# Performance work log

Hardware: AMD Instinct MI355X
Metric: run time of the kernel (lower is better)

## Reference

```python
import jax, jax.numpy as jnp
import numpy as np

N, E, FN, FE, H, L, S = 50000, 800000, 16, 8, 64, 3, 32

def layernorm(h, g, b, eps=1e-5):
    mu = h.mean(-1, keepdims=True)
    var = ((h - mu) ** 2).mean(-1, keepdims=True)
    return (h - mu) / jnp.sqrt(var + eps) * g + b

def setup_inputs() -> dict:
    key = jax.random.key(0)
    ks = iter(jax.random.split(key, 64))
    nrm = lambda shape: jax.random.normal(next(ks), shape, jnp.float32) * 0.05
    inp = {}
    inp['x'] = jax.random.normal(next(ks), (N, FN), jnp.float32)
    inp['edge_index'] = jax.random.randint(next(ks), (2, E), 0, N)
    inp['edge_attr'] = jax.random.normal(next(ks), (E, FE), jnp.float32)
    # node / edge encoders: Linear -> ReLU -> LayerNorm
    inp['Wn'] = nrm((FN, H)); inp['bn'] = jnp.zeros((H,)); inp['gn'] = jnp.ones((H,)); inp['betan'] = jnp.zeros((H,))
    inp['We'] = nrm((FE, H)); inp['be'] = jnp.zeros((H,)); inp['ge'] = jnp.ones((H,)); inp['betae'] = jnp.zeros((H,))
    # EdgeConv MLPs (stacked over layers): Linear(2H,H) -> ReLU -> Linear(H,H)
    inp['Wc1'] = nrm((L, 2 * H, H)); inp['bc1'] = jnp.zeros((L, H))
    inp['Wc2'] = nrm((L, H, H)); inp['bc2'] = jnp.zeros((L, H))
    # GATConv (heads=1): lin weight, att_src, att_dst, bias
    inp['Wg'] = nrm((L, H, H)); inp['att_src'] = nrm((L, H)); inp['att_dst'] = nrm((L, H)); inp['bg'] = jnp.zeros((L, H))
    # q predictor
    inp['Wq1'] = nrm((H, H)); inp['bq1'] = jnp.zeros((H,)); inp['gq'] = jnp.ones((H,)); inp['betaq'] = jnp.zeros((H,))
    inp['Wq2'] = nrm((H, S)); inp['bq2'] = jnp.zeros((S,))
    # value predictor
    inp['Wv1'] = nrm((H, H)); inp['bv1'] = jnp.zeros((H,)); inp['gv'] = jnp.ones((H,)); inp['betav'] = jnp.zeros((H,))
    inp['Wv2'] = nrm((H, 1)); inp['bv2'] = jnp.zeros((1,))
    return inp

def reference(x, edge_index, edge_attr, Wn, bn, gn, betan, We, be, ge, betae,
              Wc1, bc1, Wc2, bc2, Wg, att_src, att_dst, bg,
              Wq1, bq1, gq, betaq, Wq2, bq2, Wv1, bv1, gv, betav, Wv2, bv2):
    n = x.shape[0]
    src, dst = edge_index[0], edge_index[1]  # PyG: row=source(j), col=target(i)
    h = layernorm(jax.nn.relu(x @ Wn + bn), gn, betan)
    _ea = layernorm(jax.nn.relu(edge_attr @ We + be), ge, betae)  # encoded but unused by EdgeConv message (faithful)
    loop = jnp.arange(n)
    gsrc = jnp.concatenate([src, loop])  # GAT adds self-loops
    gdst = jnp.concatenate([dst, loop])
    for l in range(L):
        # EdgeConv: gather x_i (target), x_j (source), concat, MLP, scatter-max at target
        m = jnp.concatenate([h[dst], h[src]], axis=1)  # [E, 2H]
        m = jax.nn.relu(m @ Wc1[l] + bc1[l]) @ Wc2[l] + bc2[l]
        agg = jax.ops.segment_max(m, dst, num_segments=n)
        agg = jnp.where(jnp.isneginf(agg), 0.0, agg)  # PyG scatter-max leaves empty rows at 0
        # GATConv (1 head): alpha = softmax_i(leaky_relu(a_s.xg_j + a_d.xg_i))
        xg = h @ Wg[l]
        a_s = xg @ att_src[l]
        a_d = xg @ att_dst[l]
        e = jax.nn.leaky_relu(a_s[gsrc] + a_d[gdst], 0.2)
        emax = jax.ops.segment_max(e, gdst, num_segments=n)
        w = jnp.exp(e - emax[gdst])
        alpha = w / jax.ops.segment_sum(w, gdst, num_segments=n)[gdst]
        att = jax.ops.segment_sum(xg[gsrc] * alpha[:, None], gdst, num_segments=n) + bg[l]
        h = jax.nn.relu(h + agg + att)
    t = h[0]
    tq = layernorm(jax.nn.relu(t @ Wq1 + bq1), gq, betaq)
    q_values = tq @ Wq2 + bq2
    tv = layernorm(jax.nn.relu(t @ Wv1 + bv1), gv, betav)
    value = tv @ Wv2 + bv2
    return (q_values, value)
```

## Files before the change

kernel.cpp:

```cpp
#include <hip/hip_runtime.h>
#include <math.h>

#define N_NODES 50000
#define N_EDGES 800000
#define FN_DIM 16
#define HD 64
#define T_CAP 8192
#define T2_CAP 512
#define MAXDEG 128

__device__ __forceinline__ float wsum64(float v) {
    #pragma unroll
    for (int o = 1; o < 64; o <<= 1) v += __shfl_xor(v, o);
    return v;
}
__device__ __forceinline__ float wmax64(float v) {
    #pragma unroll
    for (int o = 1; o < 64; o <<= 1) v = fmaxf(v, __shfl_xor(v, o));
    return v;
}
__device__ __forceinline__ float lrelu02(float v) { return v > 0.f ? v : 0.2f * v; }

__global__ void k_mark2(const int* __restrict__ ei, int* need1, int* need2) {
    int e = blockIdx.x * blockDim.x + threadIdx.x;
    if (e == 0) { need1[0] = 1; need2[0] = 1; }
    if (e >= N_EDGES) return;
    if (ei[N_EDGES + e] == 0) { int s = ei[e]; need2[s] = 1; need1[s] = 1; }
}
__global__ void k_mark1(const int* __restrict__ ei, const int* __restrict__ need2, int* need1) {
    int e = blockIdx.x * blockDim.x + threadIdx.x;
    if (e >= N_EDGES) return;
    if (need2[ei[N_EDGES + e]]) need1[ei[e]] = 1;
}
__global__ void k_compact(const int* __restrict__ need1, const int* __restrict__ need2,
                          int* list1, int* list2, int* idx1, int* idx2, int* cnt) {
    int i = blockIdx.x * blockDim.x + threadIdx.x;
    if (i >= N_NODES) return;
    if (need1[i]) { int p = atomicAdd(&cnt[0], 1); if (p < T_CAP)  { list1[p] = i; idx1[i] = p; } }
    if (need2[i]) { int p = atomicAdd(&cnt[1], 1); if (p < T2_CAP) { list2[p] = i; idx2[i] = p; } }
}
__global__ void k_bucket(const int* __restrict__ ei, const int* __restrict__ need1,
                         const int* __restrict__ need2,
                         const int* __restrict__ idx1, const int* __restrict__ idx2,
                         int* eb1, int* deg1, int* eb2, int* deg2, int* eb3, int* deg3) {
    int e = blockIdx.x * blockDim.x + threadIdx.x;
    if (e >= N_EDGES) return;
    int d = ei[N_EDGES + e];
    int s = ei[e];
    if (need1[d]) {
        int t = idx1[d];
        if ((unsigned)t < T_CAP) { int p = atomicAdd(&deg1[t], 1); if (p < MAXDEG) eb1[t * MAXDEG + p] = s; }
    }
    if (need2[d]) {
        int t = idx2[d];
        if ((unsigned)t < T2_CAP) { int p = atomicAdd(&deg2[t], 1); if (p < MAXDEG) eb2[t * MAXDEG + p] = s; }
    }
    if (d == 0) { int p = atomicAdd(deg3, 1); if (p < MAXDEG) eb3[p] = s; }
}

template<int LM>
__device__ __forceinline__ float node_h(int i, int lane,
    const float* __restrict__ x, const float* __restrict__ Wn, const float* __restrict__ bn,
    const float* __restrict__ gn, const float* __restrict__ betan,
    const float* __restrict__ hin) {
    if (LM == 0) {
        float acc = bn[lane];
        #pragma unroll
        for (int k = 0; k < FN_DIM; k++) acc += x[i * FN_DIM + k] * Wn[k * HD + lane];
        float v = fmaxf(acc, 0.f);
        float mu = wsum64(v) * (1.f / 64.f);
        float d = v - mu;
        float var = wsum64(d * d) * (1.f / 64.f);
        return d * rsqrtf(var + 1e-5f) * gn[lane] + betan[lane];
    } else {
        return hin[i * HD + lane];
    }
}

__device__ __forceinline__ void heads_eval(float hv, int lane,
    const float* __restrict__ Wq1, const float* __restrict__ bq1,
    const float* __restrict__ gq, const float* __restrict__ betaq,
    const float* __restrict__ Wq2, const float* __restrict__ bq2,
    const float* __restrict__ Wv1, const float* __restrict__ bv1,
    const float* __restrict__ gv, const float* __restrict__ betav,
    const float* __restrict__ Wv2, const float* __restrict__ bv2,
    float* __restrict__ out) {
    float acc = bq1[lane];
    #pragma unroll 8
    for (int k = 0; k < 64; k++) acc += __shfl(hv, k) * Wq1[k * 64 + lane];
    float r = fmaxf(acc, 0.f);
    float mu = wsum64(r) * (1.f / 64.f);
    float d = r - mu;
    float var = wsum64(d * d) * (1.f / 64.f);
    float tq = d * rsqrtf(var + 1e-5f) * gq[lane] + betaq[lane];
    float accv = bv1[lane];
    #pragma unroll 8
    for (int k = 0; k < 64; k++) accv += __shfl(hv, k) * Wv1[k * 64 + lane];
    float rv = fmaxf(accv, 0.f);
    float muv = wsum64(rv) * (1.f / 64.f);
    float dv = rv - muv;
    float varv = wsum64(dv * dv) * (1.f / 64.f);
    float tv = dv * rsqrtf(varv + 1e-5f) * gv[lane] + betav[lane];
    int s = lane & 31;
    float q = bq2[s];
    #pragma unroll 8
    for (int k = 0; k < 64; k++) q += __shfl(tq, k) * Wq2[k * 32 + s];
    if (lane < 32) out[lane] = q;
    float vsum = wsum64(tv * Wv2[lane]);
    if (lane == 0) out[32] = vsum + bv2[0];
}

template<int LM>
__global__ __launch_bounds__(256) void k_layer(
    const float* __restrict__ x, const float* __restrict__ Wn, const float* __restrict__ bn,
    const float* __restrict__ gn, const float* __restrict__ betan,
    const float* __restrict__ hin,
    const float* __restrict__ Wc1, const float* __restrict__ bc1,
    const float* __restrict__ Wc2, const float* __restrict__ bc2,
    const float* __restrict__ Wg, const float* __restrict__ atts, const float* __restrict__ attd,
    const float* __restrict__ bgv,
    const int* __restrict__ tlist, const int* __restrict__ cntp, int tcap,
    const int* __restrict__ eb, const int* __restrict__ deg,
    float* __restrict__ hout,
    const float* __restrict__ Wq1, const float* __restrict__ bq1,
    const float* __restrict__ gq, const float* __restrict__ betaq,
    const float* __restrict__ Wq2, const float* __restrict__ bq2,
    const float* __restrict__ Wv1, const float* __restrict__ bv1,
    const float* __restrict__ gv, const float* __restrict__ betav,
    const float* __restrict__ Wv2, const float* __restrict__ bv2)
{
    __shared__ float ht[64], ut[64], xgt[64];
    __shared__ float scr[4][4][64];
    __shared__ float xgc[MAXDEG][64];
    __shared__ float ec[MAXDEG];
    __shared__ float redA[4][64], redB[4][64];
    __shared__ float sws[4];
    __shared__ float sA[2];
    __shared__ float sEm;

    int lane = threadIdx.x & 63;
    int wv = threadIdx.x >> 6;
    int ntgt = (LM == 2) ? 1 : min(cntp[0], tcap);

    for (int w = blockIdx.x; w < ntgt; w += gridDim.x) {
        int t = (LM == 2) ? 0 : tlist[w];
        if (wv == 0) {
            float h = node_h<LM>(t, lane, x, Wn, bn, gn, betan, hin);
            ht[lane] = h;
            float u = bc1[lane], xg = 0.f;
            #pragma unroll 4
            for (int k = 0; k < 64; k++) {
                float b = ht[k];
                u  += b * Wc1[k * 64 + lane];
                xg += b * Wg[k * 64 + lane];
            }
            ut[lane] = u; xgt[lane] = xg;
            float a_st = wsum64(xg * atts[lane]);
            float a_dt = wsum64(xg * attd[lane]);
            if (lane == 0) { sA[0] = a_st; sA[1] = a_dt; }
        }
        __syncthreads();
        int dg = deg[(LM == 2) ? 0 : w]; if (dg > MAXDEG) dg = MAXDEG;
        float a_dt = sA[1];
        float aggw = -INFINITY;

        for (int base = wv * 4; base < dg; base += 16) {
            int ne = dg - base; if (ne > 4) ne = 4;
            #pragma unroll
            for (int e = 0; e < 4; e++) {
                if (e < ne) {
                    int s = eb[w * MAXDEG + base + e];
                    scr[wv][e][lane] = node_h<LM>(s, lane, x, Wn, bn, gn, betan, hin);
                }
            }
            float v[4] = {0.f, 0.f, 0.f, 0.f};
            float g[4] = {0.f, 0.f, 0.f, 0.f};
            #pragma unroll 4
            for (int k = 0; k < 64; k++) {
                float wc = Wc1[(64 + k) * 64 + lane];
                float wg = Wg[k * 64 + lane];
                #pragma unroll
                for (int e = 0; e < 4; e++) {
                    float b = scr[wv][e][k];
                    v[e] += b * wc;
                    g[e] += b * wg;
                }
            }
            float ut_l = ut[lane];
            #pragma unroll
            for (int e = 0; e < 4; e++) scr[wv][e][lane] = fmaxf(ut_l + v[e], 0.f);
            float m[4];
            #pragma unroll
            for (int e = 0; e < 4; e++) m[e] = bc2[lane];
            #pragma unroll 4
            for (int k = 0; k < 64; k++) {
                float wc2v = Wc2[k * 64 + lane];
                #pragma unroll
                for (int e = 0; e < 4; e++) m[e] += scr[wv][e][k] * wc2v;
            }
            #pragma unroll
            for (int e = 0; e < 4; e++) {
                if (e < ne) {
                    aggw = fmaxf(aggw, m[e]);
                    int j = base + e;
                    xgc[j][lane] = g[e];
                    float a_ss = wsum64(g[e] * atts[lane]);
                    if (lane == 0) ec[j] = lrelu02(a_ss + a_dt);
                }
            }
        }
        redA[wv][lane] = aggw;
        __syncthreads();

        if (wv == 0) {
            float es = lrelu02(sA[0] + sA[1]);
            float mm = es;
            for (int j = lane; j < dg; j += 64) mm = fmaxf(mm, ec[j]);
            mm = wmax64(mm);
            if (lane == 0) sEm = mm;
        }
        __syncthreads();
        float em = sEm;
        float attv = 0.f, wsv = 0.f;
        for (int j = wv; j < dg; j += 4) {
            float wj = expf(ec[j] - em);
            attv += wj * xgc[j][lane];
            wsv += wj;
        }
        redB[wv][lane] = attv;
        if (lane == 0) sws[wv] = wsv;
        __syncthreads();

        if (wv == 0) {
            float agg = fmaxf(fmaxf(redA[0][lane], redA[1][lane]),
                              fmaxf(redA[2][lane], redA[3][lane]));
            if (dg == 0) agg = 0.f;
            float es = lrelu02(sA[0] + sA[1]);
            float wself = expf(es - em);
            float att = redB[0][lane] + redB[1][lane] + redB[2][lane] + redB[3][lane]
                      + wself * xgt[lane];
            float wsum = sws[0] + sws[1] + sws[2] + sws[3] + wself;
            float hv = fmaxf(ht[lane] + agg + att / wsum + bgv[lane], 0.f);
            if (LM == 2) {
                heads_eval(hv, lane, Wq1, bq1, gq, betaq, Wq2, bq2,
                           Wv1, bv1, gv, betav, Wv2, bv2, hout);
            } else {
                hout[t * HD + lane] = hv;
            }
        }
        __syncthreads();
    }
}

extern "C" void kernel_launch(void* const* d_in, const int* in_sizes, int n_in,
                              void* d_out, int out_size, void* d_ws, size_t ws_size,
                              hipStream_t stream) {
    const float* x        = (const float*)d_in[0];
    const int*   ei       = (const int*)d_in[1];
    const float* Wn       = (const float*)d_in[3];
    const float* bn       = (const float*)d_in[4];
    const float* gn       = (const float*)d_in[5];
    const float* betan    = (const float*)d_in[6];
    const float* Wc1      = (const float*)d_in[11];
    const float* bc1      = (const float*)d_in[12];
    const float* Wc2      = (const float*)d_in[13];
    const float* bc2      = (const float*)d_in[14];
    const float* Wg       = (const float*)d_in[15];
    const float* att_src  = (const float*)d_in[16];
    const float* att_dst  = (const float*)d_in[17];
    const float* bg       = (const float*)d_in[18];
    const float* Wq1      = (const float*)d_in[19];
    const float* bq1      = (const float*)d_in[20];
    const float* gq       = (const float*)d_in[21];
    const float* betaq    = (const float*)d_in[22];
    const float* Wq2      = (const float*)d_in[23];
    const float* bq2      = (const float*)d_in[24];
    const float* Wv1      = (const float*)d_in[25];
    const float* bv1      = (const float*)d_in[26];
    const float* gv       = (const float*)d_in[27];
    const float* betav    = (const float*)d_in[28];
    const float* Wv2      = (const float*)d_in[29];
    const float* bv2      = (const float*)d_in[30];

    float* hB   = (float*)d_ws;
    float* hA   = hB + (size_t)N_NODES * HD;
    int* need1  = (int*)(hA + (size_t)N_NODES * HD);
    int* need2  = need1 + N_NODES;
    int* deg1   = need2 + N_NODES;
    int* deg2   = deg1 + T_CAP;
    int* deg3   = deg2 + T2_CAP;
    int* cnt    = deg3 + 4;
    int* idx1   = cnt + 8;
    int* idx2   = idx1 + N_NODES;
    int* list1  = idx2 + N_NODES;
    int* list2  = list1 + T_CAP;
    int* eb1    = list2 + T2_CAP;
    int* eb2    = eb1 + (size_t)T_CAP * MAXDEG;
    int* eb3    = eb2 + (size_t)T2_CAP * MAXDEG;

    size_t zero_ints = (size_t)2 * N_NODES + T_CAP + T2_CAP + 12;
    hipMemsetAsync(need1, 0, zero_ints * sizeof(int), stream);

    const int EB = (N_EDGES + 255) / 256;
    const int NB = (N_NODES + 255) / 256;

    k_mark2<<<EB, 256, 0, stream>>>(ei, need1, need2);
    k_mark1<<<EB, 256, 0, stream>>>(ei, need2, need1);
    k_compact<<<NB, 256, 0, stream>>>(need1, need2, list1, list2, idx1, idx2, cnt);
    k_bucket<<<EB, 256, 0, stream>>>(ei, need1, need2, idx1, idx2,
                                     eb1, deg1, eb2, deg2, eb3, deg3);

    k_layer<0><<<512, 256, 0, stream>>>(
        x, Wn, bn, gn, betan, (const float*)nullptr,
        Wc1 + 0 * 2 * HD * HD, bc1 + 0 * HD, Wc2 + 0 * HD * HD, bc2 + 0 * HD,
        Wg + 0 * HD * HD, att_src + 0 * HD, att_dst + 0 * HD, bg + 0 * HD,
        list1, cnt + 0, T_CAP, eb1, deg1, hB,
        Wq1, bq1, gq, betaq, Wq2, bq2, Wv1, bv1, gv, betav, Wv2, bv2);

    k_layer<1><<<64, 256, 0, stream>>>(
        x, Wn, bn, gn, betan, hB,
        Wc1 + 1 * 2 * HD * HD, bc1 + 1 * HD, Wc2 + 1 * HD * HD, bc2 + 1 * HD,
        Wg + 1 * HD * HD, att_src + 1 * HD, att_dst + 1 * HD, bg + 1 * HD,
        list2, cnt + 1, T2_CAP, eb2, deg2, hA,
        Wq1, bq1, gq, betaq, Wq2, bq2, Wv1, bv1, gv, betav, Wv2, bv2);

    k_layer<2><<<1, 256, 0, stream>>>(
        x, Wn, bn, gn, betan, hA,
        Wc1 + 2 * 2 * HD * HD, bc1 + 2 * HD, Wc2 + 2 * HD * HD, bc2 + 2 * HD,
        Wg + 2 * HD * HD, att_src + 2 * HD, att_dst + 2 * HD, bg + 2 * HD,
        (const int*)nullptr, cnt + 1, 1, eb3, deg3, (float*)d_out,
        Wq1, bq1, gq, betaq, Wq2, bq2, Wv1, bv1, gv, betav, Wv2, bv2);
}
```

Baseline: 98.36 us.

## Fold GAT projection after attention aggregation and vectorize graph preprocessing

```diff
diff --git a/kernel.cpp b/kernel.cpp
--- a/kernel.cpp
+++ b/kernel.cpp
@@ -21,52 +21,89 @@
 }
 __device__ __forceinline__ float lrelu02(float v) { return v > 0.f ? v : 0.2f * v; }
 
+__global__ void k_zero(int4* __restrict__ p, int n4) {
+    int i = blockIdx.x * blockDim.x + threadIdx.x;
+    if (i < n4) p[i] = make_int4(0, 0, 0, 0);
+}
+
 __global__ void k_mark2(const int* __restrict__ ei, int* need1, int* need2) {
-    int e = blockIdx.x * blockDim.x + threadIdx.x;
-    if (e == 0) { need1[0] = 1; need2[0] = 1; }
-    if (e >= N_EDGES) return;
-    if (ei[N_EDGES + e] == 0) { int s = ei[e]; need2[s] = 1; need1[s] = 1; }
+    int i = blockIdx.x * blockDim.x + threadIdx.x;
+    if (i == 0) { need1[0] = 1; need2[0] = 1; }
+    if (i >= N_EDGES / 4) return;
+    int4 d4 = ((const int4*)(ei + N_EDGES))[i];
+    int4 s4 = ((const int4*)ei)[i];
+    if (d4.x == 0) { need2[s4.x] = 1; need1[s4.x] = 1; }
+    if (d4.y == 0) { need2[s4.y] = 1; need1[s4.y] = 1; }
+    if (d4.z == 0) { need2[s4.z] = 1; need1[s4.z] = 1; }
+    if (d4.w == 0) { need2[s4.w] = 1; need1[s4.w] = 1; }
 }
 __global__ void k_mark1(const int* __restrict__ ei, const int* __restrict__ need2, int* need1) {
-    int e = blockIdx.x * blockDim.x + threadIdx.x;
-    if (e >= N_EDGES) return;
-    if (need2[ei[N_EDGES + e]]) need1[ei[e]] = 1;
-}
+    int i = blockIdx.x * blockDim.x + threadIdx.x;
+    if (i >= N_EDGES / 4) return;
+    int4 d4 = ((const int4*)(ei + N_EDGES))[i];
+    int4 s4 = ((const int4*)ei)[i];
+    if (need2[d4.x]) need1[s4.x] = 1;
+    if (need2[d4.y]) need1[s4.y] = 1;
+    if (need2[d4.z]) need1[s4.z] = 1;
+    if (need2[d4.w]) need1[s4.w] = 1;
+}
+
 __global__ void k_compact(const int* __restrict__ need1, const int* __restrict__ need2,
-                          int* list1, int* list2, int* idx1, int* idx2, int* cnt) {
-    int i = blockIdx.x * blockDim.x + threadIdx.x;
-    if (i >= N_NODES) return;
-    if (need1[i]) { int p = atomicAdd(&cnt[0], 1); if (p < T_CAP)  { list1[p] = i; idx1[i] = p; } }
-    if (need2[i]) { int p = atomicAdd(&cnt[1], 1); if (p < T2_CAP) { list2[p] = i; idx2[i] = p; } }
-}
+                          int* list1, int* list2, int* idx1, int* idx2, int* cnt,
+                          const float* __restrict__ Wg, const float* __restrict__ atts,
+                          const float* __restrict__ attd, float* __restrict__ pvec) {
+    int i = blockIdx.x * blockDim.x + threadIdx.x;
+    if (i < N_NODES) {
+        if (need1[i]) { int p = atomicAdd(&cnt[0], 1); if (p < T_CAP)  { list1[p] = i; idx1[i] = p; } }
+        if (need2[i]) { int p = atomicAdd(&cnt[1], 1); if (p < T2_CAP) { list2[p] = i; idx2[i] = p; } }
+    }
+    if (blockIdx.x < 6 && threadIdx.x < 64) {
+        int task = blockIdx.x; int l = task >> 1; int which = task & 1;
+        const float* att = which ? attd : atts;
+        float av = att[l * 64 + threadIdx.x];
+        const float* wg = Wg + l * 4096 + threadIdx.x * 64;
+        float acc = 0.f;
+        #pragma unroll 8
+        for (int c = 0; c < 64; c++) acc += wg[c] * __shfl(av, c);
+        pvec[l * 128 + which * 64 + threadIdx.x] = acc;
+    }
+}
+
 __global__ void k_bucket(const int* __restrict__ ei, const int* __restrict__ need1,
                          const int* __restrict__ need2,
                          const int* __restrict__ idx1, const int* __restrict__ idx2,
                          int* eb1, int* deg1, int* eb2, int* deg2, int* eb3, int* deg3) {
-    int e = blockIdx.x * blockDim.x + threadIdx.x;
-    if (e >= N_EDGES) return;
-    int d = ei[N_EDGES + e];
-    int s = ei[e];
-    if (need1[d]) {
-        int t = idx1[d];
-        if ((unsigned)t < T_CAP) { int p = atomicAdd(&deg1[t], 1); if (p < MAXDEG) eb1[t * MAXDEG + p] = s; }
-    }
-    if (need2[d]) {
-        int t = idx2[d];
-        if ((unsigned)t < T2_CAP) { int p = atomicAdd(&deg2[t], 1); if (p < MAXDEG) eb2[t * MAXDEG + p] = s; }
-    }
-    if (d == 0) { int p = atomicAdd(deg3, 1); if (p < MAXDEG) eb3[p] = s; }
+    int i = blockIdx.x * blockDim.x + threadIdx.x;
+    if (i >= N_EDGES / 4) return;
+    int4 d4 = ((const int4*)(ei + N_EDGES))[i];
+    int4 s4 = ((const int4*)ei)[i];
+    int ds[4] = {d4.x, d4.y, d4.z, d4.w};
+    int ss[4] = {s4.x, s4.y, s4.z, s4.w};
+    #pragma unroll
+    for (int c = 0; c < 4; c++) {
+        int d = ds[c], s = ss[c];
+        if (need1[d]) {
+            int t = idx1[d];
+            if ((unsigned)t < T_CAP) { int p = atomicAdd(&deg1[t], 1); if (p < MAXDEG) eb1[t * MAXDEG + p] = s; }
+        }
+        if (need2[d]) {
+            int t = idx2[d];
+            if ((unsigned)t < T2_CAP) { int p = atomicAdd(&deg2[t], 1); if (p < MAXDEG) eb2[t * MAXDEG + p] = s; }
+        }
+        if (d == 0) { int p = atomicAdd(deg3, 1); if (p < MAXDEG) eb3[p] = s; }
+    }
 }
 
 template<int LM>
-__device__ __forceinline__ float node_h(int i, int lane,
+__device__ __forceinline__ float node_h1(int i, int lane,
     const float* __restrict__ x, const float* __restrict__ Wn, const float* __restrict__ bn,
     const float* __restrict__ gn, const float* __restrict__ betan,
     const float* __restrict__ hin) {
     if (LM == 0) {
+        float xv = x[i * FN_DIM + (lane & 15)];
         float acc = bn[lane];
         #pragma unroll
-        for (int k = 0; k < FN_DIM; k++) acc += x[i * FN_DIM + k] * Wn[k * HD + lane];
+        for (int k = 0; k < FN_DIM; k++) acc += __shfl(xv, k) * Wn[k * HD + lane];
         float v = fmaxf(acc, 0.f);
         float mu = wsum64(v) * (1.f / 64.f);
         float d = v - mu;
@@ -77,47 +114,14 @@
     }
 }
 
-__device__ __forceinline__ void heads_eval(float hv, int lane,
-    const float* __restrict__ Wq1, const float* __restrict__ bq1,
-    const float* __restrict__ gq, const float* __restrict__ betaq,
-    const float* __restrict__ Wq2, const float* __restrict__ bq2,
-    const float* __restrict__ Wv1, const float* __restrict__ bv1,
-    const float* __restrict__ gv, const float* __restrict__ betav,
-    const float* __restrict__ Wv2, const float* __restrict__ bv2,
-    float* __restrict__ out) {
-    float acc = bq1[lane];
-    #pragma unroll 8
-    for (int k = 0; k < 64; k++) acc += __shfl(hv, k) * Wq1[k * 64 + lane];
-    float r = fmaxf(acc, 0.f);
-    float mu = wsum64(r) * (1.f / 64.f);
-    float d = r - mu;
-    float var = wsum64(d * d) * (1.f / 64.f);
-    float tq = d * rsqrtf(var + 1e-5f) * gq[lane] + betaq[lane];
-    float accv = bv1[lane];
-    #pragma unroll 8
-    for (int k = 0; k < 64; k++) accv += __shfl(hv, k) * Wv1[k * 64 + lane];
-    float rv = fmaxf(accv, 0.f);
-    float muv = wsum64(rv) * (1.f / 64.f);
-    float dv = rv - muv;
-    float varv = wsum64(dv * dv) * (1.f / 64.f);
-    float tv = dv * rsqrtf(varv + 1e-5f) * gv[lane] + betav[lane];
-    int s = lane & 31;
-    float q = bq2[s];
-    #pragma unroll 8
-    for (int k = 0; k < 64; k++) q += __shfl(tq, k) * Wq2[k * 32 + s];
-    if (lane < 32) out[lane] = q;
-    float vsum = wsum64(tv * Wv2[lane]);
-    if (lane == 0) out[32] = vsum + bv2[0];
-}
-
 template<int LM>
-__global__ __launch_bounds__(256) void k_layer(
+__global__ __launch_bounds__(256, 1) void k_layer(
     const float* __restrict__ x, const float* __restrict__ Wn, const float* __restrict__ bn,
     const float* __restrict__ gn, const float* __restrict__ betan,
     const float* __restrict__ hin,
     const float* __restrict__ Wc1, const float* __restrict__ bc1,
     const float* __restrict__ Wc2, const float* __restrict__ bc2,
-    const float* __restrict__ Wg, const float* __restrict__ atts, const float* __restrict__ attd,
+    const float* __restrict__ Wg, const float* __restrict__ pvec,
     const float* __restrict__ bgv,
     const int* __restrict__ tlist, const int* __restrict__ cntp, int tcap,
     const int* __restrict__ eb, const int* __restrict__ deg,
@@ -129,91 +133,95 @@
     const float* __restrict__ gv, const float* __restrict__ betav,
     const float* __restrict__ Wv2, const float* __restrict__ bv2)
 {
-    __shared__ float ht[64], ut[64], xgt[64];
-    __shared__ float scr[4][4][64];
-    __shared__ float xgc[MAXDEG][64];
+    __shared__ float hsc[MAXDEG][HD];
     __shared__ float ec[MAXDEG];
-    __shared__ float redA[4][64], redB[4][64];
+    __shared__ float redA[4][HD];
+    __shared__ float redH[4][HD];
     __shared__ float sws[4];
-    __shared__ float sA[2];
+    __shared__ float sOut[HD];
     __shared__ float sEm;
 
     int lane = threadIdx.x & 63;
     int wv = threadIdx.x >> 6;
     int ntgt = (LM == 2) ? 1 : min(cntp[0], tcap);
+    float ps = pvec[lane], pd = pvec[64 + lane];
 
     for (int w = blockIdx.x; w < ntgt; w += gridDim.x) {
         int t = (LM == 2) ? 0 : tlist[w];
-        if (wv == 0) {
-            float h = node_h<LM>(t, lane, x, Wn, bn, gn, betan, hin);
-            ht[lane] = h;
-            float u = bc1[lane], xg = 0.f;
-            #pragma unroll 4
-            for (int k = 0; k < 64; k++) {
-                float b = ht[k];
-                u  += b * Wc1[k * 64 + lane];
-                xg += b * Wg[k * 64 + lane];
-            }
-            ut[lane] = u; xgt[lane] = xg;
-            float a_st = wsum64(xg * atts[lane]);
-            float a_dt = wsum64(xg * attd[lane]);
-            if (lane == 0) { sA[0] = a_st; sA[1] = a_dt; }
-        }
-        __syncthreads();
+        float hval = node_h1<LM>(t, lane, x, Wn, bn, gn, betan, hin);
+        float uval = bc1[lane];
+        #pragma unroll 8
+        for (int k = 0; k < HD; k++) uval += __shfl(hval, k) * Wc1[k * HD + lane];
+        float a_st = wsum64(hval * ps);
+        float a_dt = wsum64(hval * pd);
+        float es = lrelu02(a_st + a_dt);
+
         int dg = deg[(LM == 2) ? 0 : w]; if (dg > MAXDEG) dg = MAXDEG;
-        float a_dt = sA[1];
         float aggw = -INFINITY;
 
         for (int base = wv * 4; base < dg; base += 16) {
             int ne = dg - base; if (ne > 4) ne = 4;
+            float hs[4] = {0.f, 0.f, 0.f, 0.f};
+            if (LM == 0) {
+                float xv[4] = {0.f, 0.f, 0.f, 0.f};
+                #pragma unroll
+                for (int e = 0; e < 4; e++)
+                    if (e < ne) xv[e] = x[eb[w * MAXDEG + base + e] * FN_DIM + (lane & 15)];
+                #pragma unroll
+                for (int e = 0; e < 4; e++) hs[e] = bn[lane];
+                #pragma unroll
+                for (int k = 0; k < FN_DIM; k++) {
+                    float wn = Wn[k * HD + lane];
+                    #pragma unroll
+                    for (int e = 0; e < 4; e++) hs[e] += __shfl(xv[e], k) * wn;
+                }
+                #pragma unroll
+                for (int e = 0; e < 4; e++) {
+                    float v = fmaxf(hs[e], 0.f);
+                    float mu = wsum64(v) * (1.f / 64.f);
+                    float d = v - mu;
+                    float var = wsum64(d * d) * (1.f / 64.f);
+                    hs[e] = d * rsqrtf(var + 1e-5f) * gn[lane] + betan[lane];
+                }
+            } else {
+                #pragma unroll
+                for (int e = 0; e < 4; e++)
+                    if (e < ne) hs[e] = hin[eb[w * MAXDEG + base + e] * HD + lane];
+            }
             #pragma unroll
             for (int e = 0; e < 4; e++) {
                 if (e < ne) {
-                    int s = eb[w * MAXDEG + base + e];
-                    scr[wv][e][lane] = node_h<LM>(s, lane, x, Wn, bn, gn, betan, hin);
+                    hsc[base + e][lane] = hs[e];
+                    float as = wsum64(hs[e] * ps);
+                    if (lane == 0) ec[base + e] = lrelu02(as + a_dt);
                 }
             }
             float v[4] = {0.f, 0.f, 0.f, 0.f};
-            float g[4] = {0.f, 0.f, 0.f, 0.f};
-            #pragma unroll 4
-            for (int k = 0; k < 64; k++) {
-                float wc = Wc1[(64 + k) * 64 + lane];
-                float wg = Wg[k * 64 + lane];
-                #pragma unroll
-                for (int e = 0; e < 4; e++) {
-                    float b = scr[wv][e][k];
-                    v[e] += b * wc;
-                    g[e] += b * wg;
-                }
-            }
-            float ut_l = ut[lane];
+            #pragma unroll 8
+            for (int k = 0; k < HD; k++) {
+                float wc = Wc1[(HD + k) * HD + lane];
+                #pragma unroll
+                for (int e = 0; e < 4; e++) v[e] += __shfl(hs[e], k) * wc;
+            }
+            float hid[4];
             #pragma unroll
-            for (int e = 0; e < 4; e++) scr[wv][e][lane] = fmaxf(ut_l + v[e], 0.f);
+            for (int e = 0; e < 4; e++) hid[e] = fmaxf(uval + v[e], 0.f);
             float m[4];
             #pragma unroll
             for (int e = 0; e < 4; e++) m[e] = bc2[lane];
-            #pragma unroll 4
-            for (int k = 0; k < 64; k++) {
-                float wc2v = Wc2[k * 64 + lane];
-                #pragma unroll
-                for (int e = 0; e < 4; e++) m[e] += scr[wv][e][k] * wc2v;
+            #pragma unroll 8
+            for (int k = 0; k < HD; k++) {
+                float wc2v = Wc2[k * HD + lane];
+                #pragma unroll
+                for (int e = 0; e < 4; e++) m[e] += __shfl(hid[e], k) * wc2v;
             }
             #pragma unroll
-            for (int e = 0; e < 4; e++) {
-                if (e < ne) {
-                    aggw = fmaxf(aggw, m[e]);
-                    int j = base + e;
-                    xgc[j][lane] = g[e];
-                    float a_ss = wsum64(g[e] * atts[lane]);
-                    if (lane == 0) ec[j] = lrelu02(a_ss + a_dt);
-                }
-            }
+            for (int e = 0; e < 4; e++) if (e < ne) aggw = fmaxf(aggw, m[e]);
         }
         redA[wv][lane] = aggw;
         __syncthreads();
 
         if (wv == 0) {
-            float es = lrelu02(sA[0] + sA[1]);
             float mm = es;
             for (int j = lane; j < dg; j += 64) mm = fmaxf(mm, ec[j]);
             mm = wmax64(mm);
@@ -221,31 +229,60 @@
         }
         __syncthreads();
         float em = sEm;
-        float attv = 0.f, wsv = 0.f;
+
+        float hw = 0.f, wsv = 0.f;
         for (int j = wv; j < dg; j += 4) {
             float wj = expf(ec[j] - em);
-            attv += wj * xgc[j][lane];
+            hw += wj * hsc[j][lane];
             wsv += wj;
         }
-        redB[wv][lane] = attv;
+        redH[wv][lane] = hw;
         if (lane == 0) sws[wv] = wsv;
         __syncthreads();
 
         if (wv == 0) {
+            float wself = expf(es - em);
+            float wsumT = sws[0] + sws[1] + sws[2] + sws[3] + wself;
+            float hbar = (redH[0][lane] + redH[1][lane] + redH[2][lane] + redH[3][lane]
+                          + wself * hval) / wsumT;
+            float att = bgv[lane];
+            #pragma unroll 8
+            for (int k = 0; k < HD; k++) att += __shfl(hbar, k) * Wg[k * HD + lane];
             float agg = fmaxf(fmaxf(redA[0][lane], redA[1][lane]),
                               fmaxf(redA[2][lane], redA[3][lane]));
             if (dg == 0) agg = 0.f;
-            float es = lrelu02(sA[0] + sA[1]);
-            float wself = expf(es - em);
-            float att = redB[0][lane] + redB[1][lane] + redB[2][lane] + redB[3][lane]
-                      + wself * xgt[lane];
-            float wsum = sws[0] + sws[1] + sws[2] + sws[3] + wself;
-            float hv = fmaxf(ht[lane] + agg + att / wsum + bgv[lane], 0.f);
-            if (LM == 2) {
-                heads_eval(hv, lane, Wq1, bq1, gq, betaq, Wq2, bq2,
-                           Wv1, bv1, gv, betav, Wv2, bv2, hout);
-            } else {
-                hout[t * HD + lane] = hv;
+            float hv = fmaxf(hval + agg + att, 0.f);
+            if (LM == 2) sOut[lane] = hv;
+            else hout[t * HD + lane] = hv;
+        }
+        if (LM == 2) {
+            __syncthreads();
+            float hvv = sOut[lane];
+            if (wv == 0) {
+                float acc = bq1[lane];
+                #pragma unroll 8
+                for (int k = 0; k < 64; k++) acc += __shfl(hvv, k) * Wq1[k * 64 + lane];
+                float r = fmaxf(acc, 0.f);
+                float mu = wsum64(r) * (1.f / 64.f);
+                float d = r - mu;
+                float var = wsum64(d * d) * (1.f / 64.f);
+                float tq = d * rsqrtf(var + 1e-5f) * gq[lane] + betaq[lane];
+                int s2 = lane & 31;
+                float q = bq2[s2];
+                #pragma unroll 8
+                for (int k = 0; k < 64; k++) q += __shfl(tq, k) * Wq2[k * 32 + s2];
+                if (lane < 32) hout[lane] = q;
+            } else if (wv == 1) {
+                float accv = bv1[lane];
+                #pragma unroll 8
+                for (int k = 0; k < 64; k++) accv += __shfl(hvv, k) * Wv1[k * 64 + lane];
+                float rv = fmaxf(accv, 0.f);
+                float muv = wsum64(rv) * (1.f / 64.f);
+                float dv = rv - muv;
+                float varv = wsum64(dv * dv) * (1.f / 64.f);
+                float tv = dv * rsqrtf(varv + 1e-5f) * gv[lane] + betav[lane];
+                float vsum = wsum64(tv * Wv2[lane]);
+                if (lane == 0) hout[32] = vsum + bv2[0];
             }
         }
         __syncthreads();
@@ -297,37 +334,39 @@
     int* eb1    = list2 + T2_CAP;
     int* eb2    = eb1 + (size_t)T_CAP * MAXDEG;
     int* eb3    = eb2 + (size_t)T2_CAP * MAXDEG;
-
-    size_t zero_ints = (size_t)2 * N_NODES + T_CAP + T2_CAP + 12;
-    hipMemsetAsync(need1, 0, zero_ints * sizeof(int), stream);
-
-    const int EB = (N_EDGES + 255) / 256;
+    float* pvec = (float*)(eb3 + MAXDEG);
+
+    const int zero_ints = 2 * N_NODES + T_CAP + T2_CAP + 12;
+    const int n4 = zero_ints / 4;
+    const int E4B = (N_EDGES / 4 + 255) / 256;
     const int NB = (N_NODES + 255) / 256;
 
-    k_mark2<<<EB, 256, 0, stream>>>(ei, need1, need2);
-    k_mark1<<<EB, 256, 0, stream>>>(ei, need2, need1);
-    k_compact<<<NB, 256, 0, stream>>>(need1, need2, list1, list2, idx1, idx2, cnt);
-    k_bucket<<<EB, 256, 0, stream>>>(ei, need1, need2, idx1, idx2,
-                                     eb1, deg1, eb2, deg2, eb3, deg3);
-
-    k_layer<0><<<512, 256, 0, stream>>>(
+    k_zero<<<(n4 + 255) / 256, 256, 0, stream>>>((int4*)need1, n4);
+    k_mark2<<<E4B, 256, 0, stream>>>(ei, need1, need2);
+    k_mark1<<<E4B, 256, 0, stream>>>(ei, need2, need1);
+    k_compact<<<NB, 256, 0, stream>>>(need1, need2, list1, list2, idx1, idx2, cnt,
+                                      Wg, att_src, att_dst, pvec);
+    k_bucket<<<E4B, 256, 0, stream>>>(ei, need1, need2, idx1, idx2,
+                                      eb1, deg1, eb2, deg2, eb3, deg3);
+
+    k_layer<0><<<320, 256, 0, stream>>>(
         x, Wn, bn, gn, betan, (const float*)nullptr,
         Wc1 + 0 * 2 * HD * HD, bc1 + 0 * HD, Wc2 + 0 * HD * HD, bc2 + 0 * HD,
-        Wg + 0 * HD * HD, att_src + 0 * HD, att_dst + 0 * HD, bg + 0 * HD,
+        Wg + 0 * HD * HD, pvec + 0 * 128, bg + 0 * HD,
         list1, cnt + 0, T_CAP, eb1, deg1, hB,
         Wq1, bq1, gq, betaq, Wq2, bq2, Wv1, bv1, gv, betav, Wv2, bv2);
 
-    k_layer<1><<<64, 256, 0, stream>>>(
+    k_layer<1><<<32, 256, 0, stream>>>(
         x, Wn, bn, gn, betan, hB,
         Wc1 + 1 * 2 * HD * HD, bc1 + 1 * HD, Wc2 + 1 * HD * HD, bc2 + 1 * HD,
-        Wg + 1 * HD * HD, att_src + 1 * HD, att_dst + 1 * HD, bg + 1 * HD,
+        Wg + 1 * HD * HD, pvec + 1 * 128, bg + 1 * HD,
         list2, cnt + 1, T2_CAP, eb2, deg2, hA,
         Wq1, bq1, gq, betaq, Wq2, bq2, Wv1, bv1, gv, betav, Wv2, bv2);
 
     k_layer<2><<<1, 256, 0, stream>>>(
         x, Wn, bn, gn, betan, hA,
         Wc1 + 2 * 2 * HD * HD, bc1 + 2 * HD, Wc2 + 2 * HD * HD, bc2 + 2 * HD,
-        Wg + 2 * HD * HD, att_src + 2 * HD, att_dst + 2 * HD, bg + 2 * HD,
+        Wg + 2 * HD * HD, pvec + 2 * 128, bg + 2 * HD,
         (const int*)nullptr, cnt + 1, 1, eb3, deg3, (float*)d_out,
         Wq1, bq1, gq, betaq, Wq2, bq2, Wv1, bv1, gv, betav, Wv2, bv2);
 }
```

Result: slower. 115.3 us (+17.3%).
